# Kernel optimization log

Hardware: AMD Instinct MI355X
Metric: run time of the kernel (lower is better)

The kernel has to match this reference:

```python
import jax, jax.numpy as jnp
import numpy as np

N_NODES = 100000
N_EDGES = 1600000
D = 32  # atom and bond feature dim


def _mlp(x, W1, b1, W2, b2, W3, b3):
    # fff: Linear(in,128) -> ReLU -> Linear(128,64) -> ReLU -> Linear(64,32)
    h = jax.nn.relu(x @ W1 + b1)
    h = jax.nn.relu(h @ W2 + b2)
    return h @ W3 + b3


def _init_mlp(key, in_dim):
    ks = jax.random.split(key, 3)
    def lin(k, fan_in, fan_out):
        bound = 1.0 / np.sqrt(fan_in)
        kw, kb = jax.random.split(k)
        W = jax.random.uniform(kw, (fan_in, fan_out), jnp.float32, -bound, bound)
        b = jax.random.uniform(kb, (fan_out,), jnp.float32, -bound, bound)
        return W, b
    W1, b1 = lin(ks[0], in_dim, 128)
    W2, b2 = lin(ks[1], 128, 64)
    W3, b3 = lin(ks[2], 64, 32)
    return W1, b1, W2, b2, W3, b3


def setup_inputs() -> dict:
    key = jax.random.key(0)
    k_bonds, k_a1, k_a2, k_atoms, k_e, k_v = jax.random.split(key, 6)
    inp = {
        "bonds": jax.random.normal(k_bonds, (N_EDGES, D), jnp.float32),
        "bond_atom_1": jax.random.randint(k_a1, (N_EDGES,), 0, N_NODES, jnp.int64),
        "bond_atom_2": jax.random.randint(k_a2, (N_EDGES,), 0, N_NODES, jnp.int64),
        "atoms": jax.random.normal(k_atoms, (N_NODES, D), jnp.float32),
    }
    We1, be1, We2, be2, We3, be3 = _init_mlp(k_e, 96)
    Wv1, bv1, Wv2, bv2, Wv3, bv3 = _init_mlp(k_v, 64)
    inp.update(We1=We1, be1=be1, We2=We2, be2=be2, We3=We3, be3=be3,
               Wv1=Wv1, bv1=bv1, Wv2=Wv2, bv2=bv2, Wv3=Wv3, bv3=bv3)
    return inp


def reference(bonds, bond_atom_1, bond_atom_2, atoms,
              We1, be1, We2, be2, We3, be3,
              Wv1, bv1, Wv2, bv2, Wv3, bv3):
    # Edge update: gather endpoint atom features, concat with bond feats, MLP
    atom1 = atoms[bond_atom_1]                    # [E, D]
    atom2 = atoms[bond_atom_2]                    # [E, D]
    e_in = jnp.concatenate([atom1, atom2, bonds], axis=1)  # [E, 3D]
    new_bonds = _mlp(e_in, We1, be1, We2, be2, We3, be3)    # [E, 32]

    # Node update: scatter-mean new bond features onto target atoms
    # (PyG default flow aggregates messages at edge_index[1] == bond_atom_2)
    n = atoms.shape[0]
    seg_sum = jax.ops.segment_sum(new_bonds, bond_atom_2, num_segments=n)
    counts = jax.ops.segment_sum(jnp.ones((new_bonds.shape[0],), new_bonds.dtype),
                                 bond_atom_2, num_segments=n)
    mean_bonds = seg_sum / jnp.maximum(counts, 1.0)[:, None]  # [N, 32]

    v_in = jnp.concatenate([mean_bonds, atoms], axis=1)        # [N, 64]
    new_atoms = _mlp(v_in, Wv1, bv1, Wv2, bv2, Wv3, bv3)       # [N, 32]
    return (new_atoms, new_bonds)
```

## Files before the change

kernel.cpp:

```cpp
#include <hip/hip_runtime.h>
#include <hip/hip_bf16.h>

#define NN 100000
#define NE 1600000
#define NB_SCAN 391
#define ETILES 12500
#define EGRID 512
#define NGRID 512

typedef __attribute__((ext_vector_type(8))) short bfrag8;
typedef __attribute__((ext_vector_type(4))) float f32x4;
typedef __attribute__((ext_vector_type(8))) unsigned short us8;
typedef __attribute__((ext_vector_type(4))) unsigned int u32x4;

__device__ __forceinline__ unsigned short f2bf(float f) {
  unsigned int u = __float_as_uint(f);
  u += 0x7fffu + ((u >> 16) & 1u);
  return (unsigned short)(u >> 16);
}

__device__ __forceinline__ unsigned int pk2(float a, float b) {
  unsigned int r;
  asm("v_cvt_pk_bf16_f32 %0, %1, %2" : "=v"(r) : "v"(a), "v"(b));
  return r;
}

__device__ __forceinline__ uint2 pk4(float v0, float v1, float v2, float v3) {
  return make_uint2(pk2(v0, v1), pk2(v2, v3));
}

__device__ __forceinline__ bfrag8 pack8(float4 a, float4 b) {
  union { u32x4 u; bfrag8 f; } c;
  c.u[0] = pk2(a.x, a.y); c.u[1] = pk2(a.z, a.w);
  c.u[2] = pk2(b.x, b.y); c.u[3] = pk2(b.z, b.w);
  return c.f;
}

__device__ __forceinline__ bfrag8 as_frag(us8 v) {
  union { us8 u; bfrag8 f; } c;
  c.u = v;
  return c.f;
}

__device__ __forceinline__ f32x4 mfma16(bfrag8 a, bfrag8 b, f32x4 c) {
  return __builtin_amdgcn_mfma_f32_16x16x32_bf16(a, b, c, 0, 0, 0);
}

__device__ __forceinline__ void gload_lds16(const void* g, void* l) {
  __builtin_amdgcn_global_load_lds(
      (const __attribute__((address_space(1))) unsigned int*)g,
      (__attribute__((address_space(3))) unsigned int*)l, 16, 0, 0);
}

__global__ void cvt_atoms(const float* __restrict__ src, unsigned short* __restrict__ dst) {
  int i = blockIdx.x * 256 + threadIdx.x;
  float4 v = *(const float4*)(src + (size_t)i * 4);
  *(uint2*)(dst + (size_t)i * 4) = pk4(v.x, v.y, v.z, v.w);
}

__global__ void pack_w(const float* __restrict__ src, unsigned short* __restrict__ dst,
                       int K, int N) {
  int i = blockIdx.x * 256 + threadIdx.x;
  if (i >= K * N) return;
  int j = i & 7;
  int gc = i >> 3;
  int c = gc % N;
  int g = gc / N;
  dst[i] = f2bf(src[(g * 8 + j) * N + c]);
}

__global__ void count_k(const int* __restrict__ a2, int* __restrict__ cnt) {
  int e = blockIdx.x * 256 + threadIdx.x;
  if (e < NE) atomicAdd(&cnt[a2[e]], 1);
}

__global__ void scan_blocks(const int* __restrict__ cnt, int* __restrict__ off,
                            int* __restrict__ bsum) {
  __shared__ int s[256];
  const int t = threadIdx.x;
  const int idx = blockIdx.x * 256 + t;
  int v = (idx < NN) ? cnt[idx] : 0;
  s[t] = v;
  __syncthreads();
  for (int d = 1; d < 256; d <<= 1) {
    int x = (t >= d) ? s[t - d] : 0;
    __syncthreads();
    s[t] += x;
    __syncthreads();
  }
  if (idx < NN) off[idx] = s[t] - v;
  if (t == 255) bsum[blockIdx.x] = s[255];
}

__global__ void scan_bsum(int* __restrict__ bsum) {
  __shared__ int s[512];
  const int t = threadIdx.x;
  int v = (t < NB_SCAN) ? bsum[t] : 0;
  s[t] = v;
  __syncthreads();
  for (int d = 1; d < 512; d <<= 1) {
    int x = (t >= d) ? s[t - d] : 0;
    __syncthreads();
    s[t] += x;
    __syncthreads();
  }
  if (t < NB_SCAN) bsum[t] = s[t] - v;
}

__global__ void scan_finalize(int* __restrict__ off, const int* __restrict__ bsum,
                              int* __restrict__ cursor) {
  int idx = blockIdx.x * 256 + threadIdx.x;
  if (idx < NN) {
    int o = off[idx] + bsum[blockIdx.x];
    off[idx] = o;
    cursor[idx] = o;
  }
  if (idx == 0) off[NN] = NE;
}

__global__ void fill_csr(const int* __restrict__ a2, int* __restrict__ cursor,
                         int* __restrict__ csr) {
  int e = blockIdx.x * 256 + threadIdx.x;
  if (e < NE) {
    int p = atomicAdd(&cursor[a2[e]], 1);
    csr[p] = e;
  }
}

__global__ __launch_bounds__(256, 2) void edge_kernel(
    const float* __restrict__ bonds, const int* __restrict__ a1p, const int* __restrict__ a2p,
    const unsigned short* __restrict__ atoms_bf,
    const float* __restrict__ be1, const float* __restrict__ be2, const float* __restrict__ be3,
    const unsigned short* __restrict__ wpack,
    float* __restrict__ new_bonds) {
  __shared__ unsigned short sW[22528];
  __shared__ float sB1[128], sB2[64], sB3[32];
  __shared__ unsigned short sH1[128 * 136];

  const int tid = threadIdx.x;
  const int lane = tid & 63, wv = tid >> 6;
  const int cl = lane & 15, q = lane >> 4;
  const int esub = wv * 32 + cl;

  {
    const char* src = (const char*)wpack;
    char* dst = (char*)sW;
#pragma unroll
    for (int i = 0; i < 11; ++i) {
      const int c = i * 4 + wv;
      gload_lds16(src + c * 1024 + lane * 16, dst + c * 1024);
    }
  }
  if (tid < 128) sB1[tid] = be1[tid];
  else if (tid < 192) sB2[tid - 128] = be2[tid - 128];
  else if (tid < 224) sB3[tid - 192] = be3[tid - 192];

  int tile = blockIdx.x;
  us8 ra1[2], ra2[2];
  float4 rb[2][2];
  int ia1n[2], ia2n[2];

#pragma unroll
  for (int t = 0; t < 2; ++t) {
    const int e = tile * 128 + esub + t * 16;
    const int ia1 = a1p[e], ia2 = a2p[e];
    ra1[t] = *(const us8*)(atoms_bf + (size_t)ia1 * 32 + q * 8);
    ra2[t] = *(const us8*)(atoms_bf + (size_t)ia2 * 32 + q * 8);
    const float* bp = bonds + (size_t)e * 32 + q * 8;
    rb[t][0] = *(const float4*)(bp);
    rb[t][1] = *(const float4*)(bp + 4);
  }
  {
    int tn = tile + EGRID; if (tn >= ETILES) tn = tile;
#pragma unroll
    for (int t = 0; t < 2; ++t) {
      const int e = tn * 128 + esub + t * 16;
      ia1n[t] = a1p[e]; ia2n[t] = a2p[e];
    }
  }
  __syncthreads();

  for (; tile < ETILES; tile += EGRID) {
    bfrag8 xb0[2], xb1[2], xb2[2];
#pragma unroll
    for (int t = 0; t < 2; ++t) {
      xb0[t] = as_frag(ra1[t]);
      xb1[t] = as_frag(ra2[t]);
      xb2[t] = pack8(rb[t][0], rb[t][1]);
    }
    const int tn = (tile + EGRID < ETILES) ? tile + EGRID : tile;
#pragma unroll
    for (int t = 0; t < 2; ++t) {
      ra1[t] = *(const us8*)(atoms_bf + (size_t)ia1n[t] * 32 + q * 8);
      ra2[t] = *(const us8*)(atoms_bf + (size_t)ia2n[t] * 32 + q * 8);
      const int e = tn * 128 + esub + t * 16;
      const float* bp = bonds + (size_t)e * 32 + q * 8;
      rb[t][0] = *(const float4*)(bp);
      rb[t][1] = *(const float4*)(bp + 4);
    }
    {
      int tnn = tile + 2 * EGRID; if (tnn >= ETILES) tnn = tn;
#pragma unroll
      for (int t = 0; t < 2; ++t) {
        const int e = tnn * 128 + esub + t * 16;
        ia1n[t] = a1p[e]; ia2n[t] = a2p[e];
      }
    }

#pragma unroll
    for (int rt = 0; rt < 8; ++rt) {
      const unsigned short* wa = &sW[(q * 128 + rt * 16 + cl) * 8];
      bfrag8 w0 = *(const bfrag8*)(wa);
      bfrag8 w1 = *(const bfrag8*)(wa + 4096);
      bfrag8 w2 = *(const bfrag8*)(wa + 8192);
      f32x4 acc[2];
      acc[0] = (f32x4){0.f, 0.f, 0.f, 0.f};
      acc[1] = (f32x4){0.f, 0.f, 0.f, 0.f};
#pragma unroll
      for (int t = 0; t < 2; ++t) {
        acc[t] = mfma16(w0, xb0[t], acc[t]);
        acc[t] = mfma16(w1, xb1[t], acc[t]);
        acc[t] = mfma16(w2, xb2[t], acc[t]);
      }
      const int c0 = rt * 16 + q * 4;
#pragma unroll
      for (int t = 0; t < 2; ++t) {
        uint2 hv = pk4(fmaxf(acc[t][0] + sB1[c0 + 0], 0.f),
                       fmaxf(acc[t][1] + sB1[c0 + 1], 0.f),
                       fmaxf(acc[t][2] + sB1[c0 + 2], 0.f),
                       fmaxf(acc[t][3] + sB1[c0 + 3], 0.f));
        *(uint2*)&sH1[(esub + t * 16) * 136 + c0] = hv;
      }
    }
    __syncthreads();

    bfrag8 hb[4][2];
#pragma unroll
    for (int t = 0; t < 2; ++t) {
      const unsigned short* hr = &sH1[(esub + t * 16) * 136 + q * 8];
#pragma unroll
      for (int ks = 0; ks < 4; ++ks) hb[ks][t] = *(const bfrag8*)(hr + ks * 32);
    }
    __syncthreads();

    unsigned short* sH2 = sH1;
#pragma unroll
    for (int rt = 0; rt < 4; ++rt) {
      f32x4 acc[2];
      acc[0] = (f32x4){0.f, 0.f, 0.f, 0.f};
      acc[1] = (f32x4){0.f, 0.f, 0.f, 0.f};
#pragma unroll
      for (int ks = 0; ks < 4; ++ks) {
        bfrag8 w = *(const bfrag8*)&sW[12288 + ks * 2048 + (q * 64 + rt * 16 + cl) * 8];
#pragma unroll
        for (int t = 0; t < 2; ++t) acc[t] = mfma16(w, hb[ks][t], acc[t]);
      }
      const int c0 = rt * 16 + q * 4;
#pragma unroll
      for (int t = 0; t < 2; ++t) {
        uint2 hv = pk4(fmaxf(acc[t][0] + sB2[c0 + 0], 0.f),
                       fmaxf(acc[t][1] + sB2[c0 + 1], 0.f),
                       fmaxf(acc[t][2] + sB2[c0 + 2], 0.f),
                       fmaxf(acc[t][3] + sB2[c0 + 3], 0.f));
        *(uint2*)&sH2[(esub + t * 16) * 72 + c0] = hv;
      }
    }
    __syncthreads();

    bfrag8 gb0[2], gb1[2];
#pragma unroll
    for (int t = 0; t < 2; ++t) {
      const unsigned short* hr = &sH2[(esub + t * 16) * 72 + q * 8];
      gb0[t] = *(const bfrag8*)(hr);
      gb1[t] = *(const bfrag8*)(hr + 32);
    }
#pragma unroll
    for (int rt = 0; rt < 2; ++rt) {
      bfrag8 w0 = *(const bfrag8*)&sW[20480 + (q * 32 + rt * 16 + cl) * 8];
      bfrag8 w1 = *(const bfrag8*)&sW[20480 + 1024 + (q * 32 + rt * 16 + cl) * 8];
      const int c0 = rt * 16 + q * 4;
#pragma unroll
      for (int t = 0; t < 2; ++t) {
        f32x4 acc = {0.f, 0.f, 0.f, 0.f};
        acc = mfma16(w0, gb0[t], acc);
        acc = mfma16(w1, gb1[t], acc);
        const int e = tile * 128 + esub + t * 16;
        float4 o;
        o.x = acc[0] + sB3[c0 + 0];
        o.y = acc[1] + sB3[c0 + 1];
        o.z = acc[2] + sB3[c0 + 2];
        o.w = acc[3] + sB3[c0 + 3];
        *(float4*)(new_bonds + (size_t)e * 32 + c0) = o;
      }
    }
    __syncthreads();
  }
}

__global__ __launch_bounds__(256, 2) void node_kernel(
    const unsigned short* __restrict__ atoms_bf,
    const float* __restrict__ bv1, const float* __restrict__ bv2, const float* __restrict__ bv3,
    const unsigned short* __restrict__ wpack,
    const int* __restrict__ off, const int* __restrict__ csr,
    const float* __restrict__ new_bonds, float* __restrict__ new_atoms) {
  __shared__ unsigned short sW[18432];
  __shared__ float sB1[128], sB2[64], sB3[32];
  __shared__ unsigned short sV[64 * 72];
  __shared__ unsigned short sH1[64 * 136];

  const int tid = threadIdx.x;
  const int lane = tid & 63, wv = tid >> 6;
  const int cl = lane & 15, q = lane >> 4;
  const int nl = tid >> 2, l4 = tid & 3;

  {
    const uint4* src = (const uint4*)wpack;
    uint4* dst = (uint4*)sW;
#pragma unroll
    for (int i = 0; i < 9; ++i) dst[tid + i * 256] = src[tid + i * 256];
  }
  if (tid < 128) sB1[tid] = bv1[tid];
  if (tid < 64) sB2[tid] = bv2[tid];
  if (tid < 32) sB3[tid] = bv3[tid];

  for (int n0 = blockIdx.x * 64; n0 < NN; n0 += NGRID * 64) {
    __syncthreads();

    {
      const int n = n0 + nl;
      unsigned short* vd = &sV[nl * 72 + l4 * 8];
      if (n < NN) {
        const int o0 = off[n], o1 = off[n + 1];
        float4 sa0 = {0.f, 0.f, 0.f, 0.f}, sa1 = {0.f, 0.f, 0.f, 0.f};
        float4 sb0 = {0.f, 0.f, 0.f, 0.f}, sb1 = {0.f, 0.f, 0.f, 0.f};
        int i = o0;
        for (; i + 1 < o1; i += 2) {
          const int ea = csr[i], eb = csr[i + 1];
          const float4* pa = (const float4*)(new_bonds + (size_t)ea * 32 + l4 * 8);
          const float4* pb = (const float4*)(new_bonds + (size_t)eb * 32 + l4 * 8);
          float4 a0 = pa[0], a1 = pa[1];
          float4 b0 = pb[0], b1 = pb[1];
          sa0.x += a0.x; sa0.y += a0.y; sa0.z += a0.z; sa0.w += a0.w;
          sa1.x += a1.x; sa1.y += a1.y; sa1.z += a1.z; sa1.w += a1.w;
          sb0.x += b0.x; sb0.y += b0.y; sb0.z += b0.z; sb0.w += b0.w;
          sb1.x += b1.x; sb1.y += b1.y; sb1.z += b1.z; sb1.w += b1.w;
        }
        if (i < o1) {
          const int ea = csr[i];
          const float4* pa = (const float4*)(new_bonds + (size_t)ea * 32 + l4 * 8);
          float4 a0 = pa[0], a1 = pa[1];
          sa0.x += a0.x; sa0.y += a0.y; sa0.z += a0.z; sa0.w += a0.w;
          sa1.x += a1.x; sa1.y += a1.y; sa1.z += a1.z; sa1.w += a1.w;
        }
        const float inv = 1.0f / fmaxf((float)(o1 - o0), 1.0f);
        uint4 m;
        m.x = pk2((sa0.x + sb0.x) * inv, (sa0.y + sb0.y) * inv);
        m.y = pk2((sa0.z + sb0.z) * inv, (sa0.w + sb0.w) * inv);
        m.z = pk2((sa1.x + sb1.x) * inv, (sa1.y + sb1.y) * inv);
        m.w = pk2((sa1.z + sb1.z) * inv, (sa1.w + sb1.w) * inv);
        *(uint4*)vd = m;
        *(us8*)&sV[nl * 72 + 32 + l4 * 8] =
            *(const us8*)(atoms_bf + (size_t)n * 32 + l4 * 8);
      } else {
        us8 z = {0, 0, 0, 0, 0, 0, 0, 0};
        *(us8*)vd = z;
        *(us8*)&sV[nl * 72 + 32 + l4 * 8] = z;
      }
    }
    __syncthreads();

    const int nt = wv * 16;
    const int ng = n0 + nt + cl;

    bfrag8 vb0 = *(const bfrag8*)&sV[(nt + cl) * 72 + q * 8];
    bfrag8 vb1 = *(const bfrag8*)&sV[(nt + cl) * 72 + 32 + q * 8];
#pragma unroll
    for (int rt = 0; rt < 8; ++rt) {
      f32x4 acc = {0.f, 0.f, 0.f, 0.f};
      acc = mfma16(*(const bfrag8*)&sW[(q * 128 + rt * 16 + cl) * 8], vb0, acc);
      acc = mfma16(*(const bfrag8*)&sW[4096 + (q * 128 + rt * 16 + cl) * 8], vb1, acc);
      const int c0 = rt * 16 + q * 4;
      uint2 hv = pk4(fmaxf(acc[0] + sB1[c0 + 0], 0.f),
                     fmaxf(acc[1] + sB1[c0 + 1], 0.f),
                     fmaxf(acc[2] + sB1[c0 + 2], 0.f),
                     fmaxf(acc[3] + sB1[c0 + 3], 0.f));
      *(uint2*)&sH1[(nt + cl) * 136 + c0] = hv;
    }
    __syncthreads();

    bfrag8 hb[4];
    {
      const unsigned short* hr = &sH1[(nt + cl) * 136 + q * 8];
#pragma unroll
      for (int ks = 0; ks < 4; ++ks) hb[ks] = *(const bfrag8*)(hr + ks * 32);
    }
    __syncthreads();
#pragma unroll
    for (int rt = 0; rt < 4; ++rt) {
      f32x4 acc = {0.f, 0.f, 0.f, 0.f};
#pragma unroll
      for (int ks = 0; ks < 4; ++ks)
        acc = mfma16(*(const bfrag8*)&sW[8192 + ks * 2048 + (q * 64 + rt * 16 + cl) * 8], hb[ks], acc);
      const int c0 = rt * 16 + q * 4;
      uint2 hv = pk4(fmaxf(acc[0] + sB2[c0 + 0], 0.f),
                     fmaxf(acc[1] + sB2[c0 + 1], 0.f),
                     fmaxf(acc[2] + sB2[c0 + 2], 0.f),
                     fmaxf(acc[3] + sB2[c0 + 3], 0.f));
      *(uint2*)&sV[(nt + cl) * 72 + c0] = hv;
    }
    __syncthreads();

    bfrag8 gb0 = *(const bfrag8*)&sV[(nt + cl) * 72 + q * 8];
    bfrag8 gb1 = *(const bfrag8*)&sV[(nt + cl) * 72 + 32 + q * 8];
    if (ng < NN) {
      float* outp = new_atoms + (size_t)ng * 32;
#pragma unroll
      for (int rt = 0; rt < 2; ++rt) {
        f32x4 acc = {0.f, 0.f, 0.f, 0.f};
        acc = mfma16(*(const bfrag8*)&sW[16384 + (q * 32 + rt * 16 + cl) * 8], gb0, acc);
        acc = mfma16(*(const bfrag8*)&sW[16384 + 1024 + (q * 32 + rt * 16 + cl) * 8], gb1, acc);
        const int c0 = rt * 16 + q * 4;
        float4 o;
        o.x = acc[0] + sB3[c0 + 0];
        o.y = acc[1] + sB3[c0 + 1];
        o.z = acc[2] + sB3[c0 + 2];
        o.w = acc[3] + sB3[c0 + 3];
        *(float4*)(outp + c0) = o;
      }
    }
  }
}

extern "C" void kernel_launch(void* const* d_in, const int* in_sizes, int n_in,
                              void* d_out, int out_size, void* d_ws, size_t ws_size,
                              hipStream_t stream) {
  const float* bonds = (const float*)d_in[0];
  const int* a1 = (const int*)d_in[1];
  const int* a2 = (const int*)d_in[2];
  const float* atoms = (const float*)d_in[3];
  const float* We1 = (const float*)d_in[4];
  const float* be1 = (const float*)d_in[5];
  const float* We2 = (const float*)d_in[6];
  const float* be2 = (const float*)d_in[7];
  const float* We3 = (const float*)d_in[8];
  const float* be3 = (const float*)d_in[9];
  const float* Wv1 = (const float*)d_in[10];
  const float* bv1 = (const float*)d_in[11];
  const float* Wv2 = (const float*)d_in[12];
  const float* bv2 = (const float*)d_in[13];
  const float* Wv3 = (const float*)d_in[14];
  const float* bv3 = (const float*)d_in[15];

  float* out = (float*)d_out;
  float* new_atoms = out;
  float* new_bonds = out + (size_t)NN * 32;

  char* ws = (char*)d_ws;
  int* cnt    = (int*)(ws + 0);
  int* off    = (int*)(ws + 400000);
  int* bsum   = (int*)(ws + 800016);
  unsigned short* wp = (unsigned short*)(ws + 802064);
  int* csr    = (int*)(ws + 883984);
  unsigned short* atoms_bf = (unsigned short*)(ws + 7283984);

  hipMemsetAsync(cnt, 0, (size_t)NN * 4, stream);

  cvt_atoms<<<3125, 256, 0, stream>>>(atoms, atoms_bf);

  pack_w<<<48, 256, 0, stream>>>(We1, wp + 0, 96, 128);
  pack_w<<<32, 256, 0, stream>>>(We2, wp + 12288, 128, 64);
  pack_w<<<8, 256, 0, stream>>>(We3, wp + 20480, 64, 32);
  pack_w<<<32, 256, 0, stream>>>(Wv1, wp + 22528, 64, 128);
  pack_w<<<32, 256, 0, stream>>>(Wv2, wp + 30720, 128, 64);
  pack_w<<<8, 256, 0, stream>>>(Wv3, wp + 38912, 64, 32);

  count_k<<<(NE + 255) / 256, 256, 0, stream>>>(a2, cnt);
  scan_blocks<<<NB_SCAN, 256, 0, stream>>>(cnt, off, bsum);
  scan_bsum<<<1, 512, 0, stream>>>(bsum);
  scan_finalize<<<NB_SCAN, 256, 0, stream>>>(off, bsum, cnt);
  fill_csr<<<(NE + 255) / 256, 256, 0, stream>>>(a2, cnt, csr);

  edge_kernel<<<EGRID, 256, 0, stream>>>(bonds, a1, a2, atoms_bf, be1, be2, be3, wp,
                                         new_bonds);
  node_kernel<<<NGRID, 256, 0, stream>>>(atoms_bf, bv1, bv2, bv3, wp + 22528,
                                         off, csr, new_bonds, new_atoms);
}
```

Baseline: 437.2 us.

## Split node kernel into a separate gather-mean pass and a node MLP kernel

After: 428.3 us. -2.0%, faster.

```diff
diff --git a/kernel.cpp b/kernel.cpp
--- a/kernel.cpp
+++ b/kernel.cpp
@@ -6,7 +6,7 @@
 #define NB_SCAN 391
 #define ETILES 12500
 #define EGRID 512
-#define NGRID 512
+#define NGRID 1024
 
 typedef __attribute__((ext_vector_type(8))) short bfrag8;
 typedef __attribute__((ext_vector_type(4))) float f32x4;
@@ -297,12 +297,40 @@
   }
 }
 
-__global__ __launch_bounds__(256, 2) void node_kernel(
+__global__ __launch_bounds__(256, 4) void gather_mean(
+    const int* __restrict__ off, const int* __restrict__ csr,
+    const float* __restrict__ new_bonds, float* __restrict__ mean_f32) {
+  const int tid = blockIdx.x * 256 + threadIdx.x;
+  const int n = tid >> 3, sl = tid & 7;
+  const int o0 = off[n], o1 = off[n + 1];
+  float4 s0 = {0.f, 0.f, 0.f, 0.f}, s1 = {0.f, 0.f, 0.f, 0.f};
+  int i = o0;
+  for (; i + 1 < o1; i += 2) {
+    const int ea = csr[i], eb = csr[i + 1];
+    float4 a = *(const float4*)(new_bonds + (size_t)ea * 32 + sl * 4);
+    float4 b = *(const float4*)(new_bonds + (size_t)eb * 32 + sl * 4);
+    s0.x += a.x; s0.y += a.y; s0.z += a.z; s0.w += a.w;
+    s1.x += b.x; s1.y += b.y; s1.z += b.z; s1.w += b.w;
+  }
+  if (i < o1) {
+    const int ea = csr[i];
+    float4 a = *(const float4*)(new_bonds + (size_t)ea * 32 + sl * 4);
+    s0.x += a.x; s0.y += a.y; s0.z += a.z; s0.w += a.w;
+  }
+  const float inv = 1.0f / fmaxf((float)(o1 - o0), 1.0f);
+  float4 m;
+  m.x = (s0.x + s1.x) * inv;
+  m.y = (s0.y + s1.y) * inv;
+  m.z = (s0.z + s1.z) * inv;
+  m.w = (s0.w + s1.w) * inv;
+  *(float4*)(mean_f32 + (size_t)n * 32 + sl * 4) = m;
+}
+
+__global__ __launch_bounds__(256, 4) void node_mlp(
     const unsigned short* __restrict__ atoms_bf,
     const float* __restrict__ bv1, const float* __restrict__ bv2, const float* __restrict__ bv3,
     const unsigned short* __restrict__ wpack,
-    const int* __restrict__ off, const int* __restrict__ csr,
-    const float* __restrict__ new_bonds, float* __restrict__ new_atoms) {
+    const float* __restrict__ mean_f32, float* __restrict__ new_atoms) {
   __shared__ unsigned short sW[18432];
   __shared__ float sB1[128], sB2[64], sB3[32];
   __shared__ unsigned short sV[64 * 72];
@@ -328,43 +356,29 @@
 
     {
       const int n = n0 + nl;
-      unsigned short* vd = &sV[nl * 72 + l4 * 8];
       if (n < NN) {
-        const int o0 = off[n], o1 = off[n + 1];
-        float4 sa0 = {0.f, 0.f, 0.f, 0.f}, sa1 = {0.f, 0.f, 0.f, 0.f};
-        float4 sb0 = {0.f, 0.f, 0.f, 0.f}, sb1 = {0.f, 0.f, 0.f, 0.f};
-        int i = o0;
-        for (; i + 1 < o1; i += 2) {
-          const int ea = csr[i], eb = csr[i + 1];
-          const float4* pa = (const float4*)(new_bonds + (size_t)ea * 32 + l4 * 8);
-          const float4* pb = (const float4*)(new_bonds + (size_t)eb * 32 + l4 * 8);
-          float4 a0 = pa[0], a1 = pa[1];
-          float4 b0 = pb[0], b1 = pb[1];
-          sa0.x += a0.x; sa0.y += a0.y; sa0.z += a0.z; sa0.w += a0.w;
-          sa1.x += a1.x; sa1.y += a1.y; sa1.z += a1.z; sa1.w += a1.w;
-          sb0.x += b0.x; sb0.y += b0.y; sb0.z += b0.z; sb0.w += b0.w;
-          sb1.x += b1.x; sb1.y += b1.y; sb1.z += b1.z; sb1.w += b1.w;
+        if (l4 < 2) {
+          const float* sp = mean_f32 + (size_t)n * 32 + l4 * 16;
+          float4 a = *(const float4*)(sp);
+          float4 b = *(const float4*)(sp + 4);
+          float4 c = *(const float4*)(sp + 8);
+          float4 d = *(const float4*)(sp + 12);
+          uint4 o0, o1;
+          o0.x = pk2(a.x, a.y); o0.y = pk2(a.z, a.w);
+          o0.z = pk2(b.x, b.y); o0.w = pk2(b.z, b.w);
+          o1.x = pk2(c.x, c.y); o1.y = pk2(c.z, c.w);
+          o1.z = pk2(d.x, d.y); o1.w = pk2(d.z, d.w);
+          *(uint4*)&sV[nl * 72 + l4 * 16] = o0;
+          *(uint4*)&sV[nl * 72 + l4 * 16 + 8] = o1;
+        } else {
+          const unsigned short* ap = atoms_bf + (size_t)n * 32 + (l4 - 2) * 16;
+          *(us8*)&sV[nl * 72 + 32 + (l4 - 2) * 16] = *(const us8*)(ap);
+          *(us8*)&sV[nl * 72 + 32 + (l4 - 2) * 16 + 8] = *(const us8*)(ap + 8);
         }
-        if (i < o1) {
-          const int ea = csr[i];
-          const float4* pa = (const float4*)(new_bonds + (size_t)ea * 32 + l4 * 8);
-          float4 a0 = pa[0], a1 = pa[1];
-          sa0.x += a0.x; sa0.y += a0.y; sa0.z += a0.z; sa0.w += a0.w;
-          sa1.x += a1.x; sa1.y += a1.y; sa1.z += a1.z; sa1.w += a1.w;
-        }
-        const float inv = 1.0f / fmaxf((float)(o1 - o0), 1.0f);
-        uint4 m;
-        m.x = pk2((sa0.x + sb0.x) * inv, (sa0.y + sb0.y) * inv);
-        m.y = pk2((sa0.z + sb0.z) * inv, (sa0.w + sb0.w) * inv);
-        m.z = pk2((sa1.x + sb1.x) * inv, (sa1.y + sb1.y) * inv);
-        m.w = pk2((sa1.z + sb1.z) * inv, (sa1.w + sb1.w) * inv);
-        *(uint4*)vd = m;
-        *(us8*)&sV[nl * 72 + 32 + l4 * 8] =
-            *(const us8*)(atoms_bf + (size_t)n * 32 + l4 * 8);
       } else {
         us8 z = {0, 0, 0, 0, 0, 0, 0, 0};
-        *(us8*)vd = z;
-        *(us8*)&sV[nl * 72 + 32 + l4 * 8] = z;
+        *(us8*)&sV[nl * 72 + l4 * 16] = z;
+        *(us8*)&sV[nl * 72 + l4 * 16 + 8] = z;
       }
     }
     __syncthreads();
@@ -482,6 +496,7 @@
 
   edge_kernel<<<EGRID, 256, 0, stream>>>(bonds, a1, a2, atoms_bf, be1, be2, be3, wp,
                                          new_bonds);
-  node_kernel<<<NGRID, 256, 0, stream>>>(atoms_bf, bv1, bv2, bv3, wp + 22528,
-                                         off, csr, new_bonds, new_atoms);
-}
+  gather_mean<<<NN * 8 / 256, 256, 0, stream>>>(off, csr, new_bonds, new_atoms);
+  node_mlp<<<NGRID, 256, 0, stream>>>(atoms_bf, bv1, bv2, bv3, wp + 22528,
+                                      new_atoms , new_atoms );
+}
```
